# Optimization experiments

Measured on AMD Instinct MI355X. Metric: run time of the kernel, lower is better.

Reference implementation:

```python
import jax, jax.numpy as jnp
import numpy as np

B, T, C = 2, 2048, 2048
N_HEAD, N_KV_HEAD, HEAD_DIM = 16, 4, 128
N_REP = N_HEAD // N_KV_HEAD
EPS = 1e-05


def setup_inputs() -> dict:
    key = jax.random.key(0)
    ks = jax.random.split(key, 8)
    # rope freqs as cos/sin of theta_t,i = t / 10000^(2i/d)
    inv_freq = 1.0 / (10000.0 ** (np.arange(0, HEAD_DIM, 2, dtype=np.float32) / HEAD_DIM))
    ang = np.arange(T, dtype=np.float32)[:, None] * inv_freq[None, :]  # [T, HEAD_DIM//2]
    scale = 0.02
    return {
        "x": jax.random.normal(ks[0], (B, T, C), jnp.float32),
        "freqs_cos": jnp.asarray(np.cos(ang)),
        "freqs_sin": jnp.asarray(np.sin(ang)),
        "wq": jax.random.normal(ks[1], (C, N_HEAD * HEAD_DIM), jnp.float32) * scale,
        "wk": jax.random.normal(ks[2], (C, N_KV_HEAD * HEAD_DIM), jnp.float32) * scale,
        "wv": jax.random.normal(ks[3], (C, N_KV_HEAD * HEAD_DIM), jnp.float32) * scale,
        "wo": jax.random.normal(ks[4], (N_HEAD * HEAD_DIM, C), jnp.float32) * scale,
        "q_norm_w": jnp.ones((HEAD_DIM,), jnp.float32),
        "k_norm_w": jnp.ones((HEAD_DIM,), jnp.float32),
    }


def _rmsnorm(x, w):
    var = jnp.mean(jnp.square(x), axis=-1, keepdims=True)
    return x * jax.lax.rsqrt(var + EPS) * w


def _rope(x, cos, sin):
    # x: [B, T, H, D]; interpret last dim as interleaved (real, imag) pairs
    xr = x[..., 0::2]
    xi = x[..., 1::2]
    c = cos[None, :, None, :]
    s = sin[None, :, None, :]
    out_r = xr * c - xi * s
    out_i = xr * s + xi * c
    return jnp.stack([out_r, out_i], axis=-1).reshape(x.shape)


def reference(x, freqs_cos, freqs_sin, wq, wk, wv, wo, q_norm_w, k_norm_w):
    # QKV projections
    xq = (x @ wq).reshape(B, T, N_HEAD, HEAD_DIM)
    xk = (x @ wk).reshape(B, T, N_KV_HEAD, HEAD_DIM)
    xv = (x @ wv).reshape(B, T, N_KV_HEAD, HEAD_DIM)
    # optional q/k RMSNorm (use_qk_norm=True)
    xq = _rmsnorm(xq, q_norm_w)
    xk = _rmsnorm(xk, k_norm_w)
    # RoPE
    xq = _rope(xq, freqs_cos, freqs_sin)
    xk = _rope(xk, freqs_cos, freqs_sin)
    # GQA expand: each kv head repeated N_REP times contiguously
    xk = jnp.repeat(xk, N_REP, axis=2)  # [B, T, N_HEAD, D]
    xv = jnp.repeat(xv, N_REP, axis=2)
    # causal SDPA
    scores = jnp.einsum("bthd,bshd->bhts", xq, xk) / jnp.sqrt(jnp.float32(HEAD_DIM))
    causal = jnp.tril(jnp.ones((T, T), bool))
    scores = jnp.where(causal[None, None], scores, jnp.float32(-1e30))
    attn = jax.nn.softmax(scores, axis=-1)
    y = jnp.einsum("bhts,bshd->bthd", attn, xv).reshape(B, T, N_HEAD * HEAD_DIM)
    return y @ wo
```

## Files before the change

### kernel.cpp

```cpp
#include <hip/hip_runtime.h>
#include <hip/hip_bf16.h>

using u16 = unsigned short;
using u32 = unsigned int;

typedef short bf16x8 __attribute__((ext_vector_type(8)));
typedef float f32x4 __attribute__((ext_vector_type(4)));

#define AS1 __attribute__((address_space(1)))
#define AS3 __attribute__((address_space(3)))

__device__ __forceinline__ void gll16(const void* g, void* l) {
  __builtin_amdgcn_global_load_lds((const AS1 u32*)g, (AS3 u32*)l, 16, 0, 0);
}

__device__ __forceinline__ u16 f2bf(float x) {
  u32 u = __builtin_bit_cast(u32, x);
  u32 r = (u + 0x7fffu + ((u >> 16) & 1u)) >> 16;
  return (u16)r;
}
__device__ __forceinline__ u32 pk2(float lo, float hi) {
  return (u32)f2bf(lo) | ((u32)f2bf(hi) << 16);
}
__device__ __forceinline__ u16 f2bf_fast(float x) {
  __hip_bfloat16 h = __float2bfloat16(x);
  return __builtin_bit_cast(u16, h);
}

__device__ __forceinline__ void trans64(const float* __restrict__ in, u16* __restrict__ out,
                                        int R, int Cc, int bx, int by, float (*tl)[65]) {
  int c0 = bx * 64, r0 = by * 64, tid = threadIdx.x;
#pragma unroll
  for (int i = 0; i < 16; i++) {
    int idx = i * 256 + tid; int tr = idx >> 6, tc = idx & 63;
    tl[tr][tc] = in[(size_t)(r0 + tr) * Cc + c0 + tc];
  }
  __syncthreads();
#pragma unroll
  for (int i = 0; i < 16; i++) {
    int idx = i * 256 + tid; int tr = idx >> 6, tc = idx & 63;
    out[(size_t)(c0 + tr) * R + r0 + tc] = f2bf(tl[tc][tr]);
  }
}

__global__ void k_prep(const float* __restrict__ x, u16* __restrict__ xb,
                       const float* __restrict__ wq, u16* __restrict__ wqt,
                       const float* __restrict__ wk, const float* __restrict__ wv,
                       u16* __restrict__ wkvt,
                       const float* __restrict__ wo, u16* __restrict__ wot,
                       const float* __restrict__ fc, const float* __restrict__ fs,
                       float2* __restrict__ fcs) {
  __shared__ float tl[64][65];
  int gid = blockIdx.x;
  if (gid < 4096) {
    int i = gid * 256 + threadIdx.x;
    const float4* p = (const float4*)(x + (size_t)i * 8);
    float4 a = p[0], b = p[1];
    uint4 o;
    o.x = pk2(a.x, a.y); o.y = pk2(a.z, a.w);
    o.z = pk2(b.x, b.y); o.w = pk2(b.z, b.w);
    *(uint4*)(xb + (size_t)i * 8) = o;
  } else if (gid < 5120) {
    int t = gid - 4096; trans64(wq, wqt, 2048, 2048, t & 31, t >> 5, tl);
  } else if (gid < 5376) {
    int t = gid - 5120; trans64(wk, wkvt, 2048, 512, t & 7, t >> 3, tl);
  } else if (gid < 5632) {
    int t = gid - 5376; trans64(wv, wkvt + 512 * 2048, 2048, 512, t & 7, t >> 3, tl);
  } else if (gid < 6656) {
    int t = gid - 5632; trans64(wo, wot, 2048, 2048, t & 31, t >> 5, tl);
  } else {
    int base = (gid - 6656) * 2048 + threadIdx.x * 8;
#pragma unroll
    for (int j = 0; j < 8; j++) {
      int idx = base + j;
      fcs[idx] = make_float2(fc[idx], fs[idx]);
    }
  }
}

__global__ __launch_bounds__(512, 2) void k_gemm_qkv(
    const u16* __restrict__ A, const u16* __restrict__ BT0, const u16* __restrict__ BT1,
    u16* __restrict__ Qout, u16* __restrict__ Kout, u16* __restrict__ Vout,
    const float* __restrict__ nwq, const float* __restrict__ nwk,
    const float2* __restrict__ fcs) {
  __shared__ char lds[131072];
  const int K = 2048;
  int tid = threadIdx.x, w = tid >> 6, l = tid & 63, lg = l >> 4, ll = l & 15;
  int wr = w >> 2, wc = w & 3;
  int lid = blockIdx.y * 24 + blockIdx.x;
  int xcd = lid & 7, r = lid >> 3;
  int colg = xcd & 1, rowg = xcd >> 1;
  int bxt = colg * 12 + r % 12;
  int bm0 = (rowg * 8 + r / 12) * 128;
  bool qpath = (bxt < 16);
  const u16* BT = qpath ? BT0 : BT1;
  int bn0 = qpath ? bxt * 128 : (bxt - 16) * 128;

  auto stage = [&](int si, int kt) {
    char* Sb = lds + si * 32768;
    int k0 = kt * 64;
#pragma unroll
    for (int i = 0; i < 2; i++) {
      int base = i * 512 + (w << 6);
      int c = base + l;
      int row = c >> 3, kc = (c & 7) ^ (row & 7);
      gll16(A + (size_t)(bm0 + row) * K + k0 + kc * 8, Sb + base * 16);
      gll16(BT + (size_t)(bn0 + row) * K + k0 + kc * 8, Sb + 16384 + base * 16);
    }
  };

  f32x4 acc[4][2] = {};
  stage(0, 0); stage(1, 1); stage(2, 2);
  asm volatile("s_waitcnt vmcnt(8)" ::: "memory");
  __builtin_amdgcn_s_barrier();
  __builtin_amdgcn_sched_barrier(0);

  for (int kt = 0; kt < 32; ++kt) {
    int cs = kt & 3;
    if (kt + 3 < 32) stage((kt + 3) & 3, kt + 3);
    char* As = lds + cs * 32768;
    char* Bs = As + 16384;
    __builtin_amdgcn_s_setprio(1);
#pragma unroll
    for (int ks = 0; ks < 2; ks++) {
      bf16x8 af[4], bf[2];
#pragma unroll
      for (int m = 0; m < 4; m++) {
        int row = 64 * wr + 16 * m + ll;
        af[m] = *(const bf16x8*)(As + row * 128 + (((lg + 4 * ks) ^ (row & 7)) << 4));
      }
#pragma unroll
      for (int n = 0; n < 2; n++) {
        int row = 32 * wc + 16 * n + ll;
        bf[n] = *(const bf16x8*)(Bs + row * 128 + (((lg + 4 * ks) ^ (row & 7)) << 4));
      }
#pragma unroll
      for (int m = 0; m < 4; m++)
#pragma unroll
        for (int n = 0; n < 2; n++)
          acc[m][n] = __builtin_amdgcn_mfma_f32_16x16x32_bf16(af[m], bf[n], acc[m][n], 0, 0, 0);
    }
    __builtin_amdgcn_s_setprio(0);
    if (kt <= 28) {
      asm volatile("s_waitcnt vmcnt(8)" ::: "memory");
    } else if (kt == 29) {
      asm volatile("s_waitcnt vmcnt(4)" ::: "memory");
    } else {
      asm volatile("s_waitcnt vmcnt(0)" ::: "memory");
    }
    __builtin_amdgcn_s_barrier();
    __builtin_amdgcn_sched_barrier(0);
  }

  if (qpath || bn0 < 512) {
    const float* nw = qpath ? nwq : nwk;
    u16* O = qpath ? Qout : Kout;
    int ostride = qpath ? 2048 : 512;
    float outscale = qpath ? 0.12751744843f : 1.0f;
    float* ssum = (float*)lds;
    float ps[4][4];
#pragma unroll
    for (int m = 0; m < 4; m++)
#pragma unroll
      for (int r2 = 0; r2 < 4; r2++) {
        float p = 0.f;
#pragma unroll
        for (int n = 0; n < 2; n++) p += acc[m][n][r2] * acc[m][n][r2];
#pragma unroll
        for (int msk = 1; msk < 16; msk <<= 1) p += __shfl_xor(p, msk);
        ps[m][r2] = p;
      }
    if (ll == 0) {
#pragma unroll
      for (int m = 0; m < 4; m++)
#pragma unroll
        for (int r2 = 0; r2 < 4; r2++)
          ssum[wr * 256 + (16 * m + 4 * lg + r2) * 4 + wc] = ps[m][r2];
    }
    __syncthreads();
    float rs[4][4];
#pragma unroll
    for (int m = 0; m < 4; m++)
#pragma unroll
      for (int r2 = 0; r2 < 4; r2++) {
        int rowl = 16 * m + 4 * lg + r2;
        const float* sp = ssum + wr * 256 + rowl * 4;
        float tot = sp[0] + sp[1] + sp[2] + sp[3];
        rs[m][r2] = rsqrtf(tot * (1.0f / 128.0f) + 1e-5f) * outscale;
      }
#pragma unroll
    for (int m = 0; m < 4; m++)
#pragma unroll
      for (int n = 0; n < 2; n++) {
        int col = bn0 + 32 * wc + 16 * n + ll;
        int d = col & 127;
        float wgt = nw[d];
        int i = d >> 1;
#pragma unroll
        for (int r2 = 0; r2 < 4; r2++) {
          int row = bm0 + 64 * wr + 16 * m + 4 * lg + r2;
          int t = row & 2047;
          float y = acc[m][n][r2] * rs[m][r2] * wgt;
          float p = __shfl_xor(y, 1);
          float2 cs2 = fcs[t * 64 + i];
          float o = (ll & 1) ? (p * cs2.y + y * cs2.x) : (y * cs2.x - p * cs2.y);
          O[(size_t)row * ostride + col] = f2bf(o);
        }
      }
  } else {
    int b = bm0 >> 11, t0g = bm0 & 2047;
    int kvh = (bn0 - 512) >> 7;
    int bk = b * 4 + kvh;
#pragma unroll
    for (int m = 0; m < 4; m++)
#pragma unroll
      for (int n = 0; n < 2; n++) {
        int d = 32 * wc + 16 * n + ll;
        int tloc = 64 * wr + 16 * m + 4 * lg;
        u32 w0 = pk2(acc[m][n][0], acc[m][n][1]);
        u32 w1 = pk2(acc[m][n][2], acc[m][n][3]);
        int byte = (d * 256 + tloc * 2) ^ ((d & 7) << 4);
        *(uint2*)(lds + byte) = make_uint2(w0, w1);
      }
    __syncthreads();
    int tc = tid & 15, dbase = tid >> 4;
#pragma unroll
    for (int pass = 0; pass < 4; pass++) {
      int d = dbase + pass * 32;
      int byte = (d * 256 + tc * 16) ^ ((d & 7) << 4);
      uint4 v = *(const uint4*)(lds + byte);
      *(uint4*)(Vout + ((size_t)(bk * 128 + d)) * 2048 + t0g + tc * 8) = v;
    }
  }
}

__global__ __launch_bounds__(512, 2) void k_gemm_o(
    const u16* __restrict__ A, const u16* __restrict__ BT, float* __restrict__ C) {
  __shared__ char lds[147456];
  const int K = 2048;
  int tid = threadIdx.x, w = tid >> 6, l = tid & 63, lg = l >> 4, ll = l & 15;
  int wr = w >> 2, wc = w & 3;
  int lid = blockIdx.y * 8 + blockIdx.x;
  int xcd = lid & 7, r = lid >> 3;
  int colg = xcd & 1, rowg = xcd >> 1;
  int bxt = colg * 4 + (r & 3);
  int bm0 = (rowg * 8 + (r >> 2)) * 128;
  int bn0 = bxt * 256;

  auto stage = [&](int si, int kt) {
    char* Sb = lds + si * 49152;
    int k0 = kt * 64;
#pragma unroll
    for (int i = 0; i < 2; i++) {
      int base = i * 512 + (w << 6);
      int c = base + l;
      int row = c >> 3, kc = (c & 7) ^ (row & 7);
      gll16(A + (size_t)(bm0 + row) * K + k0 + kc * 8, Sb + base * 16);
    }
#pragma unroll
    for (int i = 0; i < 4; i++) {
      int base = i * 512 + (w << 6);
      int c = base + l;
      int row = c >> 3, kc = (c & 7) ^ (row & 7);
      gll16(BT + (size_t)(bn0 + row) * K + k0 + kc * 8, Sb + 16384 + base * 16);
    }
  };

  f32x4 acc[4][4] = {};
  stage(0, 0); stage(1, 1);
  asm volatile("s_waitcnt vmcnt(6)" ::: "memory");
  __builtin_amdgcn_s_barrier();
  __builtin_amdgcn_sched_barrier(0);

  for (int kt = 0; kt < 32; ++kt) {
    int cs = kt % 3;
    if (kt + 2 < 32) stage((kt + 2) % 3, kt + 2);
    char* As = lds + cs * 49152;
    char* Bs = As + 16384;
    __builtin_amdgcn_s_setprio(1);
#pragma unroll
    for (int ks = 0; ks < 2; ks++) {
      bf16x8 af[4], bf[4];
#pragma unroll
      for (int m = 0; m < 4; m++) {
        int row = 64 * wr + 16 * m + ll;
        af[m] = *(const bf16x8*)(As + row * 128 + (((lg + 4 * ks) ^ (row & 7)) << 4));
      }
#pragma unroll
      for (int n = 0; n < 4; n++) {
        int row = 64 * wc + 16 * n + ll;
        bf[n] = *(const bf16x8*)(Bs + row * 128 + (((lg + 4 * ks) ^ (row & 7)) << 4));
      }
#pragma unroll
      for (int m = 0; m < 4; m++)
#pragma unroll
        for (int n = 0; n < 4; n++)
          acc[m][n] = __builtin_amdgcn_mfma_f32_16x16x32_bf16(af[m], bf[n], acc[m][n], 0, 0, 0);
    }
    __builtin_amdgcn_s_setprio(0);
    if (kt + 2 < 32) {
      asm volatile("s_waitcnt vmcnt(6)" ::: "memory");
    } else {
      asm volatile("s_waitcnt vmcnt(0)" ::: "memory");
    }
    __builtin_amdgcn_s_barrier();
    __builtin_amdgcn_sched_barrier(0);
  }

#pragma unroll
  for (int m = 0; m < 4; m++)
#pragma unroll
    for (int n = 0; n < 4; n++) {
      int row = bm0 + 64 * wr + 16 * m + 4 * lg;
      int col = bn0 + 64 * wc + 16 * n + ll;
      float* cp = C + (size_t)row * 2048 + col;
#pragma unroll
      for (int r2 = 0; r2 < 4; r2++) cp[(size_t)r2 * 2048] = acc[m][n][r2];
    }
}

__global__ __launch_bounds__(512, 2) void k_attn(
    const u16* __restrict__ Q, const u16* __restrict__ Kb,
    const u16* __restrict__ Vt, u16* __restrict__ Y) {
  __shared__ char lds[81920];
  char* Ps = lds + 65536;
  int tid = threadIdx.x, w = tid >> 6, l = tid & 63, lg = l >> 4, ll = l & 15;
  int fid = blockIdx.x;
  int g = fid & 7, rank = fid >> 3;
  int b = g >> 2, kvh = g & 3;
  int h = kvh * 4 + (w & 3);
  int rgrp = w >> 2;
  const u16* Kbase = Kb + ((size_t)b * 2048) * 512 + kvh * 128;
  const u16* Vbase = Vt + ((size_t)(b * 4 + kvh) * 128) * 2048;

  const bf16x8 vones = {(short)0x3F80, (short)0x3F80, (short)0x3F80, (short)0x3F80,
                        (short)0x3F80, (short)0x3F80, (short)0x3F80, (short)0x3F80};

  auto stage = [&](int bi, int k0) {
    char* Kd = lds + (bi ? 32768 : 0);
    char* Vd = Kd + 16384;
#pragma unroll
    for (int i = 0; i < 2; i++) {
      int base = i * 512 + (w << 6);
      int c = base + l;
      int dst = base * 16;
      int krow = c >> 4, ksrc = (c & 15) ^ (krow & 7);
      gll16(Kbase + (size_t)(k0 + krow) * 512 + ksrc * 8, Kd + dst);
      int vd = c >> 3, vsrc = (c & 7) ^ (vd & 7);
      gll16(Vbase + (size_t)vd * 2048 + k0 + vsrc * 8, Vd + dst);
    }
  };

#pragma unroll 1
  for (int qi = 0; qi < 2; qi++) {
    int qt = qi ? (63 - rank) : rank;
    int q0 = qt * 32;
    int nt = (qt >> 1) + 1;
    bf16x8 qf[4];
    {
      int qrow = b * 2048 + q0 + rgrp * 16 + ll;
      const u16* qp = Q + (size_t)qrow * 2048 + h * 128;
#pragma unroll
      for (int ks = 0; ks < 4; ks++) qf[ks] = *(const bf16x8*)(qp + ks * 32 + lg * 8);
    }
    f32x4 o[8] = {};
    f32x4 lacc = {};

    stage(0, 0);
    asm volatile("s_waitcnt vmcnt(0)" ::: "memory");
    __syncthreads();

    int cur = 0;
    for (int it = 0; it < nt; ++it) {
      if (it + 1 < nt) stage(cur ^ 1, (it + 1) * 64);
      char* Ks = lds + (cur ? 32768 : 0);
      char* Vs = Ks + 16384;
      f32x4 s[4] = {};
      __builtin_amdgcn_s_setprio(1);
#pragma unroll
      for (int ks = 0; ks < 4; ks++) {
#pragma unroll
        for (int n = 0; n < 4; n++) {
          int row = 16 * n + ll;
          bf16x8 kf = *(const bf16x8*)(Ks + ((row * 256 + (lg + 4 * ks) * 16) ^ ((row & 7) << 4)));
          s[n] = __builtin_amdgcn_mfma_f32_16x16x32_bf16(qf[ks], kf, s[n], 0, 0, 0);
        }
      }
      __builtin_amdgcn_s_setprio(0);
      if (it == nt - 1) {
        int k0 = it * 64;
#pragma unroll
        for (int n = 0; n < 4; n++) {
          int kk = k0 + 16 * n + ll;
#pragma unroll
          for (int r = 0; r < 4; r++) {
            int qq = q0 + rgrp * 16 + 4 * lg + r;
            if (kk > qq) s[n][r] = -1e30f;
          }
        }
      }
#pragma unroll
      for (int r = 0; r < 4; r++) {
        int prow = 4 * lg + r;
#pragma unroll
        for (int n = 0; n < 4; n++) {
          float e = exp2f(s[n][r]);
          int byte = (w << 11) + ((prow * 128 + (16 * n + ll) * 2) ^ ((prow & 7) << 4));
          *(u16*)(Ps + byte) = f2bf_fast(e);
        }
      }
      __builtin_amdgcn_s_setprio(1);
#pragma unroll
      for (int ks = 0; ks < 2; ks++) {
        bf16x8 pf = *(const bf16x8*)(Ps + (w << 11) + ((ll * 128 + (lg + 4 * ks) * 16) ^ ((ll & 7) << 4)));
        lacc = __builtin_amdgcn_mfma_f32_16x16x32_bf16(pf, vones, lacc, 0, 0, 0);
#pragma unroll
        for (int n = 0; n < 8; n++) {
          int row = 16 * n + ll;
          bf16x8 vf = *(const bf16x8*)(Vs + ((row * 128 + (lg + 4 * ks) * 16) ^ ((row & 7) << 4)));
          o[n] = __builtin_amdgcn_mfma_f32_16x16x32_bf16(pf, vf, o[n], 0, 0, 0);
        }
      }
      __builtin_amdgcn_s_setprio(0);
      asm volatile("s_waitcnt vmcnt(0)" ::: "memory");
      __syncthreads();
      cur ^= 1;
    }
    float rl[4];
#pragma unroll
    for (int r = 0; r < 4; r++) rl[r] = 1.0f / lacc[r];
#pragma unroll
    for (int n = 0; n < 8; n++) {
      int col = h * 128 + 16 * n + ll;
#pragma unroll
      for (int r = 0; r < 4; r++) {
        int trow = b * 2048 + q0 + rgrp * 16 + 4 * lg + r;
        Y[(size_t)trow * 2048 + col] = f2bf_fast(o[n][r] * rl[r]);
      }
    }
  }
}

extern "C" void kernel_launch(void* const* d_in, const int* in_sizes, int n_in,
                              void* d_out, int out_size, void* d_ws, size_t ws_size,
                              hipStream_t stream) {
  const float* x   = (const float*)d_in[0];
  const float* fc  = (const float*)d_in[1];
  const float* fs  = (const float*)d_in[2];
  const float* wq  = (const float*)d_in[3];
  const float* wk  = (const float*)d_in[4];
  const float* wv  = (const float*)d_in[5];
  const float* wo  = (const float*)d_in[6];
  const float* qnw = (const float*)d_in[7];
  const float* knw = (const float*)d_in[8];
  float* out = (float*)d_out;

  const size_t MB = 1ull << 20;
  char* ws = (char*)d_ws;
  u16*    xb   = (u16*)(ws);
  u16*    wqt  = (u16*)(ws + 16 * MB);
  u16*    wkvt = (u16*)(ws + 24 * MB);
  u16*    wot  = (u16*)(ws + 28 * MB);
  u16*    Qb   = (u16*)(ws + 36 * MB);
  u16*    Kbq  = (u16*)(ws + 52 * MB);
  u16*    Vtg  = (u16*)(ws + 56 * MB);
  u16*    Yb   = (u16*)(ws + 60 * MB);
  float2* fcs  = (float2*)(ws + 76 * MB);

  hipLaunchKernelGGL(k_prep, dim3(6720), dim3(256), 0, stream,
                     x, xb, wq, wqt, wk, wv, wkvt, wo, wot, fc, fs, fcs);
  hipLaunchKernelGGL(k_gemm_qkv, dim3(24, 32), dim3(512), 0, stream,
                     xb, wqt, wkvt, Qb, Kbq, Vtg, qnw, knw, fcs);
  hipLaunchKernelGGL(k_attn, dim3(256), dim3(512), 0, stream, Qb, Kbq, Vtg, Yb);
  hipLaunchKernelGGL(k_gemm_o, dim3(8, 32), dim3(512), 0, stream, Yb, wot, out);
}
```

Baseline: 195.3 us.

## Use 128x256 tiles for Q projection and keep 128x128 tiles for K/V

The fused QKV GEMM now uses a 1D grid of 512 blocks. The first 256 blocks compute Q with wider 128x256 tiles and a 3-stage pipeline, which reuses each A tile across twice as many columns. The remaining 256 blocks compute K and V with the original 128x128 tiles and 4-stage pipeline. The Q path's RMSNorm partial sums now combine two waves per head instead of four. This cuts A-operand reloads and the total block count, at the cost of more LDS (147 KB), more accumulator registers, and a shallower prefetch for Q blocks.

```diff
diff --git a/kernel.cpp b/kernel.cpp
--- a/kernel.cpp
+++ b/kernel.cpp
@@ -83,80 +83,79 @@
     u16* __restrict__ Qout, u16* __restrict__ Kout, u16* __restrict__ Vout,
     const float* __restrict__ nwq, const float* __restrict__ nwk,
     const float2* __restrict__ fcs) {
-  __shared__ char lds[131072];
+  __shared__ char lds[147456];
   const int K = 2048;
   int tid = threadIdx.x, w = tid >> 6, l = tid & 63, lg = l >> 4, ll = l & 15;
-  int wr = w >> 2, wc = w & 3;
-  int lid = blockIdx.y * 24 + blockIdx.x;
-  int xcd = lid & 7, r = lid >> 3;
-  int colg = xcd & 1, rowg = xcd >> 1;
-  int bxt = colg * 12 + r % 12;
-  int bm0 = (rowg * 8 + r / 12) * 128;
-  bool qpath = (bxt < 16);
-  const u16* BT = qpath ? BT0 : BT1;
-  int bn0 = qpath ? bxt * 128 : (bxt - 16) * 128;
-
-  auto stage = [&](int si, int kt) {
-    char* Sb = lds + si * 32768;
-    int k0 = kt * 64;
-#pragma unroll
-    for (int i = 0; i < 2; i++) {
-      int base = i * 512 + (w << 6);
-      int c = base + l;
-      int row = c >> 3, kc = (c & 7) ^ (row & 7);
-      gll16(A + (size_t)(bm0 + row) * K + k0 + kc * 8, Sb + base * 16);
-      gll16(BT + (size_t)(bn0 + row) * K + k0 + kc * 8, Sb + 16384 + base * 16);
-    }
-  };
-
-  f32x4 acc[4][2] = {};
-  stage(0, 0); stage(1, 1); stage(2, 2);
-  asm volatile("s_waitcnt vmcnt(8)" ::: "memory");
-  __builtin_amdgcn_s_barrier();
-  __builtin_amdgcn_sched_barrier(0);
-
-  for (int kt = 0; kt < 32; ++kt) {
-    int cs = kt & 3;
-    if (kt + 3 < 32) stage((kt + 3) & 3, kt + 3);
-    char* As = lds + cs * 32768;
-    char* Bs = As + 16384;
-    __builtin_amdgcn_s_setprio(1);
-#pragma unroll
-    for (int ks = 0; ks < 2; ks++) {
-      bf16x8 af[4], bf[2];
-#pragma unroll
-      for (int m = 0; m < 4; m++) {
-        int row = 64 * wr + 16 * m + ll;
-        af[m] = *(const bf16x8*)(As + row * 128 + (((lg + 4 * ks) ^ (row & 7)) << 4));
-      }
-#pragma unroll
-      for (int n = 0; n < 2; n++) {
-        int row = 32 * wc + 16 * n + ll;
-        bf[n] = *(const bf16x8*)(Bs + row * 128 + (((lg + 4 * ks) ^ (row & 7)) << 4));
-      }
-#pragma unroll
-      for (int m = 0; m < 4; m++)
-#pragma unroll
-        for (int n = 0; n < 2; n++)
-          acc[m][n] = __builtin_amdgcn_mfma_f32_16x16x32_bf16(af[m], bf[n], acc[m][n], 0, 0, 0);
-    }
-    __builtin_amdgcn_s_setprio(0);
-    if (kt <= 28) {
-      asm volatile("s_waitcnt vmcnt(8)" ::: "memory");
-    } else if (kt == 29) {
-      asm volatile("s_waitcnt vmcnt(4)" ::: "memory");
-    } else {
-      asm volatile("s_waitcnt vmcnt(0)" ::: "memory");
-    }
+  int bid = blockIdx.x;
+
+  if (bid < 256) {
+    int wr = w >> 2, wc = w & 3;
+    int xcd = bid & 7, r = bid >> 3;
+    int colg = xcd & 1, rowg = xcd >> 1;
+    int bxt = colg * 4 + (r & 3);
+    int bm0 = (rowg * 8 + (r >> 2)) * 128;
+    int bn0 = bxt * 256;
+
+    auto stage = [&](int si, int kt) {
+      char* Sb = lds + si * 49152;
+      int k0 = kt * 64;
+#pragma unroll
+      for (int i = 0; i < 2; i++) {
+        int base = i * 512 + (w << 6);
+        int c = base + l;
+        int row = c >> 3, kc = (c & 7) ^ (row & 7);
+        gll16(A + (size_t)(bm0 + row) * K + k0 + kc * 8, Sb + base * 16);
+      }
+#pragma unroll
+      for (int i = 0; i < 4; i++) {
+        int base = i * 512 + (w << 6);
+        int c = base + l;
+        int row = c >> 3, kc = (c & 7) ^ (row & 7);
+        gll16(BT0 + (size_t)(bn0 + row) * K + k0 + kc * 8, Sb + 16384 + base * 16);
+      }
+    };
+
+    f32x4 acc[4][4] = {};
+    stage(0, 0); stage(1, 1);
+    asm volatile("s_waitcnt vmcnt(6)" ::: "memory");
     __builtin_amdgcn_s_barrier();
     __builtin_amdgcn_sched_barrier(0);
-  }
-
-  if (qpath || bn0 < 512) {
-    const float* nw = qpath ? nwq : nwk;
-    u16* O = qpath ? Qout : Kout;
-    int ostride = qpath ? 2048 : 512;
-    float outscale = qpath ? 0.12751744843f : 1.0f;
+
+    for (int kt = 0; kt < 32; ++kt) {
+      int cs = kt % 3;
+      if (kt + 2 < 32) stage((kt + 2) % 3, kt + 2);
+      char* As = lds + cs * 49152;
+      char* Bs = As + 16384;
+      __builtin_amdgcn_s_setprio(1);
+#pragma unroll
+      for (int ks = 0; ks < 2; ks++) {
+        bf16x8 af[4], bf[4];
+#pragma unroll
+        for (int m = 0; m < 4; m++) {
+          int row = 64 * wr + 16 * m + ll;
+          af[m] = *(const bf16x8*)(As + row * 128 + (((lg + 4 * ks) ^ (row & 7)) << 4));
+        }
+#pragma unroll
+        for (int n = 0; n < 4; n++) {
+          int row = 64 * wc + 16 * n + ll;
+          bf[n] = *(const bf16x8*)(Bs + row * 128 + (((lg + 4 * ks) ^ (row & 7)) << 4));
+        }
+#pragma unroll
+        for (int m = 0; m < 4; m++)
+#pragma unroll
+          for (int n = 0; n < 4; n++)
+            acc[m][n] = __builtin_amdgcn_mfma_f32_16x16x32_bf16(af[m], bf[n], acc[m][n], 0, 0, 0);
+      }
+      __builtin_amdgcn_s_setprio(0);
+      if (kt + 2 < 32) {
+        asm volatile("s_waitcnt vmcnt(6)" ::: "memory");
+      } else {
+        asm volatile("s_waitcnt vmcnt(0)" ::: "memory");
+      }
+      __builtin_amdgcn_s_barrier();
+      __builtin_amdgcn_sched_barrier(0);
+    }
+
     float* ssum = (float*)lds;
     float ps[4][4];
 #pragma unroll
@@ -165,7 +164,7 @@
       for (int r2 = 0; r2 < 4; r2++) {
         float p = 0.f;
 #pragma unroll
-        for (int n = 0; n < 2; n++) p += acc[m][n][r2] * acc[m][n][r2];
+        for (int n = 0; n < 4; n++) p += acc[m][n][r2] * acc[m][n][r2];
 #pragma unroll
         for (int msk = 1; msk < 16; msk <<= 1) p += __shfl_xor(p, msk);
         ps[m][r2] = p;
@@ -178,6 +177,7 @@
           ssum[wr * 256 + (16 * m + 4 * lg + r2) * 4 + wc] = ps[m][r2];
     }
     __syncthreads();
+    int pbase = (wc < 2) ? 0 : 2;
     float rs[4][4];
 #pragma unroll
     for (int m = 0; m < 4; m++)
@@ -185,16 +185,16 @@
       for (int r2 = 0; r2 < 4; r2++) {
         int rowl = 16 * m + 4 * lg + r2;
         const float* sp = ssum + wr * 256 + rowl * 4;
-        float tot = sp[0] + sp[1] + sp[2] + sp[3];
-        rs[m][r2] = rsqrtf(tot * (1.0f / 128.0f) + 1e-5f) * outscale;
+        float tot = sp[pbase] + sp[pbase + 1];
+        rs[m][r2] = rsqrtf(tot * (1.0f / 128.0f) + 1e-5f) * 0.12751744843f;
       }
 #pragma unroll
     for (int m = 0; m < 4; m++)
 #pragma unroll
-      for (int n = 0; n < 2; n++) {
-        int col = bn0 + 32 * wc + 16 * n + ll;
+      for (int n = 0; n < 4; n++) {
+        int col = bn0 + 64 * wc + 16 * n + ll;
         int d = col & 127;
-        float wgt = nw[d];
+        float wgt = nwq[d];
         int i = d >> 1;
 #pragma unroll
         for (int r2 = 0; r2 < 4; r2++) {
@@ -204,32 +204,150 @@
           float p = __shfl_xor(y, 1);
           float2 cs2 = fcs[t * 64 + i];
           float o = (ll & 1) ? (p * cs2.y + y * cs2.x) : (y * cs2.x - p * cs2.y);
-          O[(size_t)row * ostride + col] = f2bf(o);
+          Qout[(size_t)row * 2048 + col] = f2bf(o);
         }
       }
   } else {
-    int b = bm0 >> 11, t0g = bm0 & 2047;
-    int kvh = (bn0 - 512) >> 7;
-    int bk = b * 4 + kvh;
-#pragma unroll
-    for (int m = 0; m < 4; m++)
-#pragma unroll
-      for (int n = 0; n < 2; n++) {
-        int d = 32 * wc + 16 * n + ll;
-        int tloc = 64 * wr + 16 * m + 4 * lg;
-        u32 w0 = pk2(acc[m][n][0], acc[m][n][1]);
-        u32 w1 = pk2(acc[m][n][2], acc[m][n][3]);
-        int byte = (d * 256 + tloc * 2) ^ ((d & 7) << 4);
-        *(uint2*)(lds + byte) = make_uint2(w0, w1);
-      }
-    __syncthreads();
-    int tc = tid & 15, dbase = tid >> 4;
-#pragma unroll
-    for (int pass = 0; pass < 4; pass++) {
-      int d = dbase + pass * 32;
-      int byte = (d * 256 + tc * 16) ^ ((d & 7) << 4);
-      uint4 v = *(const uint4*)(lds + byte);
-      *(uint4*)(Vout + ((size_t)(bk * 128 + d)) * 2048 + t0g + tc * 8) = v;
+    int wr = w >> 2, wc = w & 3;
+    int lid = bid - 256;
+    int xcd = lid & 7, r = lid >> 3;
+    int colg = xcd & 1, rowg = xcd >> 1;
+    int bxt = colg * 4 + (r & 3);
+    int bm0 = (rowg * 8 + (r >> 2)) * 128;
+    int bn0 = bxt * 128;
+    bool kpath = (bn0 < 512);
+
+    auto stage = [&](int si, int kt) {
+      char* Sb = lds + si * 32768;
+      int k0 = kt * 64;
+#pragma unroll
+      for (int i = 0; i < 2; i++) {
+        int base = i * 512 + (w << 6);
+        int c = base + l;
+        int row = c >> 3, kc = (c & 7) ^ (row & 7);
+        gll16(A + (size_t)(bm0 + row) * K + k0 + kc * 8, Sb + base * 16);
+        gll16(BT1 + (size_t)(bn0 + row) * K + k0 + kc * 8, Sb + 16384 + base * 16);
+      }
+    };
+
+    f32x4 acc[4][2] = {};
+    stage(0, 0); stage(1, 1); stage(2, 2);
+    asm volatile("s_waitcnt vmcnt(8)" ::: "memory");
+    __builtin_amdgcn_s_barrier();
+    __builtin_amdgcn_sched_barrier(0);
+
+    for (int kt = 0; kt < 32; ++kt) {
+      int cs = kt & 3;
+      if (kt + 3 < 32) stage((kt + 3) & 3, kt + 3);
+      char* As = lds + cs * 32768;
+      char* Bs = As + 16384;
+      __builtin_amdgcn_s_setprio(1);
+#pragma unroll
+      for (int ks = 0; ks < 2; ks++) {
+        bf16x8 af[4], bf[2];
+#pragma unroll
+        for (int m = 0; m < 4; m++) {
+          int row = 64 * wr + 16 * m + ll;
+          af[m] = *(const bf16x8*)(As + row * 128 + (((lg + 4 * ks) ^ (row & 7)) << 4));
+        }
+#pragma unroll
+        for (int n = 0; n < 2; n++) {
+          int row = 32 * wc + 16 * n + ll;
+          bf[n] = *(const bf16x8*)(Bs + row * 128 + (((lg + 4 * ks) ^ (row & 7)) << 4));
+        }
+#pragma unroll
+        for (int m = 0; m < 4; m++)
+#pragma unroll
+          for (int n = 0; n < 2; n++)
+            acc[m][n] = __builtin_amdgcn_mfma_f32_16x16x32_bf16(af[m], bf[n], acc[m][n], 0, 0, 0);
+      }
+      __builtin_amdgcn_s_setprio(0);
+      if (kt <= 28) {
+        asm volatile("s_waitcnt vmcnt(8)" ::: "memory");
+      } else if (kt == 29) {
+        asm volatile("s_waitcnt vmcnt(4)" ::: "memory");
+      } else {
+        asm volatile("s_waitcnt vmcnt(0)" ::: "memory");
+      }
+      __builtin_amdgcn_s_barrier();
+      __builtin_amdgcn_sched_barrier(0);
+    }
+
+    if (kpath) {
+      float* ssum = (float*)lds;
+      float ps[4][4];
+#pragma unroll
+      for (int m = 0; m < 4; m++)
+#pragma unroll
+        for (int r2 = 0; r2 < 4; r2++) {
+          float p = 0.f;
+#pragma unroll
+          for (int n = 0; n < 2; n++) p += acc[m][n][r2] * acc[m][n][r2];
+#pragma unroll
+          for (int msk = 1; msk < 16; msk <<= 1) p += __shfl_xor(p, msk);
+          ps[m][r2] = p;
+        }
+      if (ll == 0) {
+#pragma unroll
+        for (int m = 0; m < 4; m++)
+#pragma unroll
+          for (int r2 = 0; r2 < 4; r2++)
+            ssum[wr * 256 + (16 * m + 4 * lg + r2) * 4 + wc] = ps[m][r2];
+      }
+      __syncthreads();
+      float rs[4][4];
+#pragma unroll
+      for (int m = 0; m < 4; m++)
+#pragma unroll
+        for (int r2 = 0; r2 < 4; r2++) {
+          int rowl = 16 * m + 4 * lg + r2;
+          const float* sp = ssum + wr * 256 + rowl * 4;
+          float tot = sp[0] + sp[1] + sp[2] + sp[3];
+          rs[m][r2] = rsqrtf(tot * (1.0f / 128.0f) + 1e-5f);
+        }
+#pragma unroll
+      for (int m = 0; m < 4; m++)
+#pragma unroll
+        for (int n = 0; n < 2; n++) {
+          int col = bn0 + 32 * wc + 16 * n + ll;
+          int d = col & 127;
+          float wgt = nwk[d];
+          int i = d >> 1;
+#pragma unroll
+          for (int r2 = 0; r2 < 4; r2++) {
+            int row = bm0 + 64 * wr + 16 * m + 4 * lg + r2;
+            int t = row & 2047;
+            float y = acc[m][n][r2] * rs[m][r2] * wgt;
+            float p = __shfl_xor(y, 1);
+            float2 cs2 = fcs[t * 64 + i];
+            float o = (ll & 1) ? (p * cs2.y + y * cs2.x) : (y * cs2.x - p * cs2.y);
+            Kout[(size_t)row * 512 + col] = f2bf(o);
+          }
+        }
+    } else {
+      int b = bm0 >> 11, t0g = bm0 & 2047;
+      int kvh = (bn0 - 512) >> 7;
+      int bk = b * 4 + kvh;
+#pragma unroll
+      for (int m = 0; m < 4; m++)
+#pragma unroll
+        for (int n = 0; n < 2; n++) {
+          int d = 32 * wc + 16 * n + ll;
+          int tloc = 64 * wr + 16 * m + 4 * lg;
+          u32 w0 = pk2(acc[m][n][0], acc[m][n][1]);
+          u32 w1 = pk2(acc[m][n][2], acc[m][n][3]);
+          int byte = (d * 256 + tloc * 2) ^ ((d & 7) << 4);
+          *(uint2*)(lds + byte) = make_uint2(w0, w1);
+        }
+      __syncthreads();
+      int tc = tid & 15, dbase = tid >> 4;
+#pragma unroll
+      for (int pass = 0; pass < 4; pass++) {
+        int d = dbase + pass * 32;
+        int byte = (d * 256 + tc * 16) ^ ((d & 7) << 4);
+        uint4 v = *(const uint4*)(lds + byte);
+        *(uint4*)(Vout + ((size_t)(bk * 128 + d)) * 2048 + t0g + tc * 8) = v;
+      }
     }
   }
 }
@@ -469,7 +587,7 @@
 
   hipLaunchKernelGGL(k_prep, dim3(6720), dim3(256), 0, stream,
                      x, xb, wq, wqt, wk, wv, wkvt, wo, wot, fc, fs, fcs);
-  hipLaunchKernelGGL(k_gemm_qkv, dim3(24, 32), dim3(512), 0, stream,
+  hipLaunchKernelGGL(k_gemm_qkv, dim3(512), dim3(512), 0, stream,
                      xb, wqt, wkvt, Qb, Kbq, Vtg, qnw, knw, fcs);
   hipLaunchKernelGGL(k_attn, dim3(256), dim3(512), 0, stream, Qb, Kbq, Vtg, Yb);
   hipLaunchKernelGGL(k_gemm_o, dim3(8, 32), dim3(512), 0, stream, Yb, wot, out);
```

New measurement: 186.4 us, median of 3. 1.05x faster.
